# Kernel tuning notes

Measured on AMD Instinct MI355X. Metric: run time of the kernel, lower is better.

## Reference

```python
import jax, jax.numpy as jnp
import numpy as np

# Dims: B=batch, T=seq, D=input=256=F*F, H=hidden=256=F*F, F=16 factor, R=16 TT rank, 4 gates (I,F,G,O)
F, R, NG = 16, 16, 4


def setup_inputs():
    key = jax.random.key(0)
    ks = jax.random.split(key, 11)
    s = 0.1  # core init scale keeps gate pre-activations O(1)
    inp = {
        "x": jax.random.normal(ks[0], (64, 1024, 256), jnp.float32),
        # TT cores for the 4 input-to-hidden gates (boundary ranks squeezed)
        "ih_g0": s * jax.random.normal(ks[1], (NG, F, R), jnp.float32),
        "ih_g1": s * jax.random.normal(ks[2], (NG, R, F, R), jnp.float32),
        "ih_g2": s * jax.random.normal(ks[3], (NG, R, F, R), jnp.float32),
        "ih_g3": s * jax.random.normal(ks[4], (NG, R, F), jnp.float32),
        "ih_bias": jnp.zeros((NG, F * F), jnp.float32),
        # TT cores for the 4 hidden-to-hidden gates
        "hh_g0": s * jax.random.normal(ks[5], (NG, F, R), jnp.float32),
        "hh_g1": s * jax.random.normal(ks[6], (NG, R, F, R), jnp.float32),
        "hh_g2": s * jax.random.normal(ks[7], (NG, R, F, R), jnp.float32),
        "hh_g3": s * jax.random.normal(ks[8], (NG, R, F), jnp.float32),
        "hh_bias": jnp.zeros((NG, F * F), jnp.float32),
    }
    return inp


def tt_linear(x2, g0, g1, g2, g3, bias):
    # x2: [N, F*F] -> contract TT cores per gate g -> [N, NG, F*F]
    n = x2.shape[0]
    x3 = x2.reshape(n, F, F)
    t = jnp.einsum('bmn,gmr->bgnr', x3, g0)      # contract first input factor
    t = jnp.einsum('bgnr,grns->bgs', t, g1)      # contract second input factor
    t = jnp.einsum('bgs,gsot->bgot', t, g2)      # emit first output factor
    y = jnp.einsum('bgot,gtp->bgop', t, g3)      # emit second output factor
    return y.reshape(n, NG, F * F) + bias        # bias: [NG, F*F]


def reference(x, ih_g0, ih_g1, ih_g2, ih_g3, ih_bias,
              hh_g0, hh_g1, hh_g2, hh_g3, hh_bias):
    B, T, D = x.shape
    H = F * F
    # Precompute input-to-hidden gate contributions for all timesteps at once
    ih_all = tt_linear(x.reshape(B * T, D), ih_g0, ih_g1, ih_g2, ih_g3, ih_bias)
    ih_all = ih_all.reshape(B, T, NG, H).transpose(1, 0, 2, 3)  # [T,B,4,H]

    def step(carry, ih_t):
        h, c = carry
        gates = ih_t + tt_linear(h, hh_g0, hh_g1, hh_g2, hh_g3, hh_bias)
        i = jax.nn.sigmoid(gates[:, 0])
        f = jax.nn.sigmoid(gates[:, 1])
        g = jnp.tanh(gates[:, 2])
        o = jax.nn.sigmoid(gates[:, 3])
        c = f * c + i * g
        h = o * jnp.tanh(c)
        return (h, c), h

    h0 = jnp.zeros((B, H), x.dtype)
    c0 = jnp.zeros((B, H), x.dtype)
    (h, c), ys = jax.lax.scan(step, (h0, c0), ih_all)
    output = ys.transpose(1, 0, 2)  # [B,T,H]
    return output, (h, c)
```

## Files before the change

### kernel.cpp

```cpp
#include <hip/hip_runtime.h>


#define WS_A1I 0
#define WS_A1H 16384
#define WS_C2I 32768
#define WS_C2H 49152
#define WS_BIAS 65536
#define WS_T2 66560

typedef float v2f __attribute__((ext_vector_type(2)));

__device__ __forceinline__ v2f pk_fma(v2f a, v2f b, v2f c) {
    v2f d;
    asm("v_pk_fma_f32 %0, %1, %2, %3" : "=v"(d) : "v"(a), "v"(b), "v"(c));
    return d;
}

__device__ __forceinline__ void bar_lds() {
    asm volatile("s_waitcnt lgkmcnt(0)\n\ts_barrier" ::: "memory");
}

template <int CTRL>
__device__ __forceinline__ float dpp_add(float v) {
    int s = __builtin_amdgcn_update_dpp(0, __float_as_int(v), CTRL, 0xF, 0xF, true);
    return v + __int_as_float(s);
}
template <int CTRL>
__device__ __forceinline__ float dpp_bcast(float v) {
    int s = __builtin_amdgcn_update_dpp(0, __float_as_int(v), CTRL, 0xF, 0xF, true);
    return __int_as_float(s);
}

__global__ void k_compose(const float* __restrict__ g0i, const float* __restrict__ g1i,
                          const float* __restrict__ g2i, const float* __restrict__ g3i,
                          const float* __restrict__ bi,
                          const float* __restrict__ g0h, const float* __restrict__ g1h,
                          const float* __restrict__ g2h, const float* __restrict__ g3h,
                          const float* __restrict__ bh,
                          float* __restrict__ ws) {
    int id = blockIdx.x * 256 + threadIdx.x;
    if (id < 16384) {
        int g = id >> 12, s = (id >> 8) & 15, mn = id & 255;
        int m = mn >> 4, n = mn & 15;
        float aI = 0.f, aH = 0.f;
        for (int r = 0; r < 16; ++r) {
            aI += g0i[(g * 16 + m) * 16 + r] * g1i[((g * 16 + r) * 16 + n) * 16 + s];
            aH += g0h[(g * 16 + m) * 16 + r] * g1h[((g * 16 + r) * 16 + n) * 16 + s];
        }
        ws[WS_A1I + (g * 16 + s) * 256 + mn] = aI;
        ws[WS_A1H + (g * 16 + s) * 256 + mn] = aH;
    } else if (id < 32768) {
        int id2 = id - 16384;
        int g = id2 >> 12, s = (id2 >> 8) & 15, j = id2 & 255;
        int o = j >> 4, p = j & 15;
        float aI = 0.f, aH = 0.f;
        for (int t = 0; t < 16; ++t) {
            aI += g2i[((g * 16 + s) * 16 + o) * 16 + t] * g3i[(g * 16 + t) * 16 + p];
            aH += g2h[((g * 16 + s) * 16 + o) * 16 + t] * g3h[(g * 16 + t) * 16 + p];
        }
        ws[WS_C2I + (g * 16 + s) * 256 + j] = aI;
        ws[WS_C2H + (g * 16 + s) * 256 + j] = aH;
    } else if (id < 33792) {
        int id2 = id - 32768;
        ws[WS_BIAS + id2] = bi[id2] + bh[id2];
    }
}

__global__ __launch_bounds__(256, 2) void k_t2ih(const float* __restrict__ x,
                                                 const float* __restrict__ ws,
                                                 float* __restrict__ T2) {
    __shared__ __align__(16) float Xs[64 * 128];
    __shared__ __align__(16) float As[64 * 128];
    const int tid = threadIdx.x;
    const long r0 = (long)blockIdx.x * 64;
    const int ro = tid & 15;
    const int q  = tid >> 4;

    const float4* X4g = (const float4*)x;
    const float4* A4  = (const float4*)(ws + WS_A1I);
    float4* Xs4 = (float4*)Xs;
    float4* As4 = (float4*)As;

    v2f acc2[4][4];
#pragma unroll
    for (int i = 0; i < 4; ++i)
#pragma unroll
        for (int j = 0; j < 4; ++j) acc2[i][j] = (v2f){0.f, 0.f};

    for (int half = 0; half < 2; ++half) {
        __syncthreads();
#pragma unroll
        for (int k = 0; k < 8; ++k) {
            int idx = k * 256 + tid;
            int row = idx >> 5, c = idx & 31;
            int sw = (row << 5) | (c ^ ((row >> 2) & 15));
            Xs4[sw] = X4g[(r0 + row) * 64 + half * 32 + c];
            As4[sw] = A4[row * 64 + half * 32 + c];
        }
        __syncthreads();

#pragma unroll 4
        for (int mn4 = 0; mn4 < 32; ++mn4) {
            float4 a[4], xv[4];
#pragma unroll
            for (int j = 0; j < 4; ++j) {
                int row = ro * 4 + j;
                a[j] = As4[(row << 5) | (mn4 ^ ro)];
            }
#pragma unroll
            for (int i = 0; i < 4; ++i) {
                int row = q * 4 + i;
                xv[i] = Xs4[(row << 5) | (mn4 ^ q)];
            }
#pragma unroll
            for (int i = 0; i < 4; ++i)
#pragma unroll
                for (int j = 0; j < 4; ++j) {
                    acc2[i][j] = pk_fma((v2f){xv[i].x, xv[i].y},
                                        (v2f){a[j].x, a[j].y}, acc2[i][j]);
                    acc2[i][j] = pk_fma((v2f){xv[i].z, xv[i].w},
                                        (v2f){a[j].z, a[j].w}, acc2[i][j]);
                }
        }
    }
#pragma unroll
    for (int i = 0; i < 4; ++i)
#pragma unroll
        for (int j = 0; j < 4; ++j)
            T2[(r0 + q * 4 + i) * 64 + ro * 4 + j] = acc2[i][j].x + acc2[i][j].y;
}

__global__ __launch_bounds__(1024, 4) void k_lstm(const float* __restrict__ ws,
                                                  const float* __restrict__ T2,
                                                  float* __restrict__ out) {
    __shared__ __align__(16) float hS[256];
    __shared__ __align__(16) float t2hS[64];
    __shared__ __align__(16) float t2iS[2][64];

    const int tid  = threadIdx.x;
    const int w    = tid >> 6;
    const int lane = tid & 63;
    const int b    = blockIdx.x;

    const int uab = 4 * w + (lane >> 4);
    const int sub = lane & 15;
    v2f a1p[8];
    {
        const float4* A1h4 = (const float4*)(ws + WS_A1H);
#pragma unroll
        for (int kk = 0; kk < 4; ++kk) {
            float4 v = A1h4[uab * 64 + sub * 4 + kk];
            a1p[2 * kk + 0] = (v2f){v.x, v.y};
            a1p[2 * kk + 1] = (v2f){v.z, v.w};
        }
    }

    const int jj = lane >> 2;
    const int g  = lane & 3;
    const int j  = 16 * w + jj;
    v2f c2hp[8], c2ip[8];
#pragma unroll
    for (int qq = 0; qq < 4; ++qq) {
        float h0 = ws[WS_C2H + (16 * g + 4 * qq + 0) * 256 + j];
        float h1 = ws[WS_C2H + (16 * g + 4 * qq + 1) * 256 + j];
        float h2 = ws[WS_C2H + (16 * g + 4 * qq + 2) * 256 + j];
        float h3 = ws[WS_C2H + (16 * g + 4 * qq + 3) * 256 + j];
        float i0 = ws[WS_C2I + (16 * g + 4 * qq + 0) * 256 + j];
        float i1 = ws[WS_C2I + (16 * g + 4 * qq + 1) * 256 + j];
        float i2 = ws[WS_C2I + (16 * g + 4 * qq + 2) * 256 + j];
        float i3 = ws[WS_C2I + (16 * g + 4 * qq + 3) * 256 + j];
        c2hp[2 * qq + 0] = (v2f){h0, h1};
        c2hp[2 * qq + 1] = (v2f){h2, h3};
        c2ip[2 * qq + 0] = (v2f){i0, i1};
        c2ip[2 * qq + 1] = (v2f){i2, i3};
    }
    float bias = ws[WS_BIAS + g * 256 + j];
    const float am = (g == 2) ? 2.0f : 1.0f;
    const float as = 1.442695040888963f * am;

#pragma unroll
    for (int i = 0; i < 8; ++i)
        asm volatile("" : "+v"(a1p[i]), "+v"(c2hp[i]), "+v"(c2ip[i]));

    const int hw = ((jj >> 2) << 6) + (w << 2) + (jj & 3);

    float c = 0.f, h_last = 0.f;
    if (tid < 256) hS[tid] = 0.f;
    const float* T2b = T2 + (long)b * 1024 * 64;
    const float4* T2b4 = (const float4*)T2b;
    float4 preA = make_float4(0.f, 0.f, 0.f, 0.f);
    float4 preB = make_float4(0.f, 0.f, 0.f, 0.f);
    if (tid < 16) {
        ((float4*)t2iS[0])[tid] = T2b4[tid];
        preA = T2b4[16 + tid];
    }
    bar_lds();

    float* outB = out + (long)b * 1024 * 256;
    const float4* hS4 = (const float4*)hS;
    const float4* th4 = (const float4*)t2hS;

    auto body = [&](int t, float4& preW, float4& preL) {
        v2f sA = (v2f){0.f, 0.f}, sB = (v2f){0.f, 0.f};
#pragma unroll
        for (int kk = 0; kk < 4; ++kk) {
            float4 hv = hS4[kk * 16 + sub];
            sA = pk_fma((v2f){hv.x, hv.y}, a1p[2 * kk + 0], sA);
            sB = pk_fma((v2f){hv.z, hv.w}, a1p[2 * kk + 1], sB);
        }
        float tv = (sA.x + sA.y) + (sB.x + sB.y);
        if ((tid < 16) && (t + 1 < 1024))
            ((float4*)t2iS[(t + 1) & 1])[tid] = preW;
        if ((tid < 16) && (t + 2 < 1024))
            preL = T2b4[(t + 2) * 16 + tid];
        tv = dpp_add<0x111>(tv);
        tv = dpp_add<0x112>(tv);
        tv = dpp_add<0x114>(tv);
        tv = dpp_add<0x118>(tv);
        if (sub == 15) t2hS[uab] = tv;

        bar_lds();

        const float4* ti4 = (const float4*)t2iS[t & 1];
        v2f aH = (v2f){bias, 0.f}, aL = (v2f){0.f, 0.f};
#pragma unroll
        for (int qq = 0; qq < 4; ++qq) {
            float4 th = th4[g * 4 + qq];
            float4 ti = ti4[g * 4 + qq];
            aH = pk_fma((v2f){th.x, th.y}, c2hp[2 * qq + 0], aH);
            aL = pk_fma((v2f){th.z, th.w}, c2hp[2 * qq + 1], aL);
            aH = pk_fma((v2f){ti.x, ti.y}, c2ip[2 * qq + 0], aH);
            aL = pk_fma((v2f){ti.z, ti.w}, c2ip[2 * qq + 1], aL);
        }
        float acc = (aH.x + aH.y) + (aL.x + aL.y);
        float e   = __builtin_amdgcn_exp2f(as * acc);
        float act = 1.0f - am * __builtin_amdgcn_rcpf(1.0f + e);
        float gi = dpp_bcast<0x00>(act);
        float gf = dpp_bcast<0x55>(act);
        float gg = dpp_bcast<0xAA>(act);
        float go = dpp_bcast<0xFF>(act);
        c = gf * c + gi * gg;
        float e2 = __builtin_amdgcn_exp2f(2.885390081777926f * c);
        float th_ = 1.0f - 2.0f * __builtin_amdgcn_rcpf(1.0f + e2);
        float h = go * th_;
        h_last = h;
        if (g == 0) {
            hS[hw] = h;
            outB[t * 256 + j] = h;
        }

        bar_lds();
    };

    for (int t = 0; t < 1024; t += 2) {
        body(t, preA, preB);
        body(t + 1, preB, preA);
    }

    if (g == 0) {
        out[16777216 + b * 256 + j] = h_last;
        out[16777216 + 16384 + b * 256 + j] = c;
    }
}

extern "C" void kernel_launch(void* const* d_in, const int* in_sizes, int n_in,
                              void* d_out, int out_size, void* d_ws, size_t ws_size,
                              hipStream_t stream) {
    const float* x     = (const float*)d_in[0];
    const float* ih_g0 = (const float*)d_in[1];
    const float* ih_g1 = (const float*)d_in[2];
    const float* ih_g2 = (const float*)d_in[3];
    const float* ih_g3 = (const float*)d_in[4];
    const float* ih_b  = (const float*)d_in[5];
    const float* hh_g0 = (const float*)d_in[6];
    const float* hh_g1 = (const float*)d_in[7];
    const float* hh_g2 = (const float*)d_in[8];
    const float* hh_g3 = (const float*)d_in[9];
    const float* hh_b  = (const float*)d_in[10];
    float* out = (float*)d_out;
    float* ws  = (float*)d_ws;

    k_compose<<<132, 256, 0, stream>>>(ih_g0, ih_g1, ih_g2, ih_g3, ih_b,
                                       hh_g0, hh_g1, hh_g2, hh_g3, hh_b, ws);
    k_t2ih<<<1024, 256, 0, stream>>>(x, ws, ws + WS_T2);
    k_lstm<<<64, 1024, 0, stream>>>(ws, ws + WS_T2, out);
}
```

Baseline: 868.4 us.

## Restructure input projection GEMM to per-wave row tiles with uniform weight loads

Rewrites the x-by-A1 projection so each wavefront owns 64 rows, one row per lane, staging x in a padded per-wave LDS tile. Each lane holds 64 accumulators, and the weight matrix is read through wave-uniform addresses that can become scalar loads. This removes the block-wide barriers and the weight staging in LDS. The grid shrinks to 256 blocks, and the cost is heavy register pressure from 64 accumulators plus many scalar/global weight reads per k-step, which may hurt occupancy.

```diff
diff --git a/kernel.cpp b/kernel.cpp
--- a/kernel.cpp
+++ b/kernel.cpp
@@ -69,65 +69,47 @@
 __global__ __launch_bounds__(256, 2) void k_t2ih(const float* __restrict__ x,
                                                  const float* __restrict__ ws,
                                                  float* __restrict__ T2) {
-    __shared__ __align__(16) float Xs[64 * 128];
-    __shared__ __align__(16) float As[64 * 128];
-    const int tid = threadIdx.x;
-    const long r0 = (long)blockIdx.x * 64;
-    const int ro = tid & 15;
-    const int q  = tid >> 4;
+    __shared__ __align__(16) float Xc[4][64 * 66 + 8];
+    const int tid  = threadIdx.x;
+    const int wv   = tid >> 6;
+    const int lane = tid & 63;
+    const long tile = (long)blockIdx.x * 4 + wv;
+    const long r0   = tile * 64;
+    float* Xw = Xc[wv];
 
     const float4* X4g = (const float4*)x;
-    const float4* A4  = (const float4*)(ws + WS_A1I);
-    float4* Xs4 = (float4*)Xs;
-    float4* As4 = (float4*)As;
-
-    v2f acc2[4][4];
-#pragma unroll
-    for (int i = 0; i < 4; ++i)
-#pragma unroll
-        for (int j = 0; j < 4; ++j) acc2[i][j] = (v2f){0.f, 0.f};
-
-    for (int half = 0; half < 2; ++half) {
-        __syncthreads();
-#pragma unroll
-        for (int k = 0; k < 8; ++k) {
-            int idx = k * 256 + tid;
-            int row = idx >> 5, c = idx & 31;
-            int sw = (row << 5) | (c ^ ((row >> 2) & 15));
-            Xs4[sw] = X4g[(r0 + row) * 64 + half * 32 + c];
-            As4[sw] = A4[row * 64 + half * 32 + c];
-        }
-        __syncthreads();
-
-#pragma unroll 4
-        for (int mn4 = 0; mn4 < 32; ++mn4) {
-            float4 a[4], xv[4];
-#pragma unroll
-            for (int j = 0; j < 4; ++j) {
-                int row = ro * 4 + j;
-                a[j] = As4[(row << 5) | (mn4 ^ ro)];
+    const float* A = ws + WS_A1I;
+
+    float acc[64];
+#pragma unroll
+    for (int u = 0; u < 64; ++u) acc[u] = 0.f;
+
+    for (int kc = 0; kc < 4; ++kc) {
+#pragma unroll
+        for (int it = 0; it < 16; ++it) {
+            int row = it * 4 + (lane >> 4);
+            int c4  = lane & 15;
+            float4 v = X4g[(r0 + row) * 64 + kc * 16 + c4];
+            float* d = &Xw[row * 66 + c4 * 4];
+            d[0] = v.x; d[1] = v.y; d[2] = v.z; d[3] = v.w;
+        }
+        for (int kp = 0; kp < 32; ++kp) {
+            v2f xp = *(const v2f*)&Xw[lane * 66 + 2 * kp];
+            const float* Ak = A + kc * 64 + 2 * kp;
+#pragma unroll
+            for (int u = 0; u < 64; ++u) {
+                acc[u] += xp.x * Ak[u * 256] + xp.y * Ak[u * 256 + 1];
             }
-#pragma unroll
-            for (int i = 0; i < 4; ++i) {
-                int row = q * 4 + i;
-                xv[i] = Xs4[(row << 5) | (mn4 ^ q)];
-            }
-#pragma unroll
-            for (int i = 0; i < 4; ++i)
-#pragma unroll
-                for (int j = 0; j < 4; ++j) {
-                    acc2[i][j] = pk_fma((v2f){xv[i].x, xv[i].y},
-                                        (v2f){a[j].x, a[j].y}, acc2[i][j]);
-                    acc2[i][j] = pk_fma((v2f){xv[i].z, xv[i].w},
-                                        (v2f){a[j].z, a[j].w}, acc2[i][j]);
-                }
-        }
-    }
-#pragma unroll
-    for (int i = 0; i < 4; ++i)
-#pragma unroll
-        for (int j = 0; j < 4; ++j)
-            T2[(r0 + q * 4 + i) * 64 + ro * 4 + j] = acc2[i][j].x + acc2[i][j].y;
+        }
+    }
+    float4* T24 = (float4*)T2;
+#pragma unroll
+    for (int u4 = 0; u4 < 16; ++u4) {
+        float4 o;
+        o.x = acc[4 * u4 + 0]; o.y = acc[4 * u4 + 1];
+        o.z = acc[4 * u4 + 2]; o.w = acc[4 * u4 + 3];
+        T24[(r0 + lane) * 16 + u4] = o;
+    }
 }
 
 __global__ __launch_bounds__(1024, 4) void k_lstm(const float* __restrict__ ws,
@@ -282,6 +264,6 @@
 
     k_compose<<<132, 256, 0, stream>>>(ih_g0, ih_g1, ih_g2, ih_g3, ih_b,
                                        hh_g0, hh_g1, hh_g2, hh_g3, hh_b, ws);
-    k_t2ih<<<1024, 256, 0, stream>>>(x, ws, ws + WS_T2);
+    k_t2ih<<<256, 256, 0, stream>>>(x, ws, ws + WS_T2);
     k_lstm<<<64, 1024, 0, stream>>>(ws, ws + WS_T2, out);
 }
```

New measurement: 1.045 ms. 1.2x slower.

## Halve LSTM block size, give each thread two hidden units

Applied to the files above, without the earlier changes.

The recurrent LSTM kernel now runs 512 threads per block instead of 1024, and each thread handles two hidden outputs and two rank-projection rows (j and j+128, uab and uab+32). Per-thread register weights double. The point is to make the per-step barriers cheaper with fewer waves and to add instruction-level parallelism inside the serial time loop. The trade-off is more serial work per thread on the critical path and higher register pressure.

```diff
diff --git a/kernel.cpp b/kernel.cpp
--- a/kernel.cpp
+++ b/kernel.cpp
@@ -130,9 +130,9 @@
             T2[(r0 + q * 4 + i) * 64 + ro * 4 + j] = acc2[i][j].x + acc2[i][j].y;
 }
 
-__global__ __launch_bounds__(1024, 4) void k_lstm(const float* __restrict__ ws,
-                                                  const float* __restrict__ T2,
-                                                  float* __restrict__ out) {
+__global__ __launch_bounds__(512, 2) void k_lstm(const float* __restrict__ ws,
+                                                 const float* __restrict__ T2,
+                                                 float* __restrict__ out) {
     __shared__ __align__(16) float hS[256];
     __shared__ __align__(16) float t2hS[64];
     __shared__ __align__(16) float t2iS[2][64];
@@ -144,47 +144,54 @@
 
     const int uab = 4 * w + (lane >> 4);
     const int sub = lane & 15;
-    v2f a1p[8];
+    v2f a1p0[8], a1p1[8];
     {
         const float4* A1h4 = (const float4*)(ws + WS_A1H);
 #pragma unroll
         for (int kk = 0; kk < 4; ++kk) {
-            float4 v = A1h4[uab * 64 + sub * 4 + kk];
-            a1p[2 * kk + 0] = (v2f){v.x, v.y};
-            a1p[2 * kk + 1] = (v2f){v.z, v.w};
+            float4 v0 = A1h4[uab * 64 + sub * 4 + kk];
+            float4 v1 = A1h4[(uab + 32) * 64 + sub * 4 + kk];
+            a1p0[2 * kk + 0] = (v2f){v0.x, v0.y};
+            a1p0[2 * kk + 1] = (v2f){v0.z, v0.w};
+            a1p1[2 * kk + 0] = (v2f){v1.x, v1.y};
+            a1p1[2 * kk + 1] = (v2f){v1.z, v1.w};
         }
     }
 
     const int jj = lane >> 2;
     const int g  = lane & 3;
-    const int j  = 16 * w + jj;
-    v2f c2hp[8], c2ip[8];
+    const int j0 = 16 * w + jj;
+    const int j1 = j0 + 128;
+    v2f c2hp0[8], c2ip0[8], c2hp1[8], c2ip1[8];
 #pragma unroll
     for (int qq = 0; qq < 4; ++qq) {
-        float h0 = ws[WS_C2H + (16 * g + 4 * qq + 0) * 256 + j];
-        float h1 = ws[WS_C2H + (16 * g + 4 * qq + 1) * 256 + j];
-        float h2 = ws[WS_C2H + (16 * g + 4 * qq + 2) * 256 + j];
-        float h3 = ws[WS_C2H + (16 * g + 4 * qq + 3) * 256 + j];
-        float i0 = ws[WS_C2I + (16 * g + 4 * qq + 0) * 256 + j];
-        float i1 = ws[WS_C2I + (16 * g + 4 * qq + 1) * 256 + j];
-        float i2 = ws[WS_C2I + (16 * g + 4 * qq + 2) * 256 + j];
-        float i3 = ws[WS_C2I + (16 * g + 4 * qq + 3) * 256 + j];
-        c2hp[2 * qq + 0] = (v2f){h0, h1};
-        c2hp[2 * qq + 1] = (v2f){h2, h3};
-        c2ip[2 * qq + 0] = (v2f){i0, i1};
-        c2ip[2 * qq + 1] = (v2f){i2, i3};
-    }
-    float bias = ws[WS_BIAS + g * 256 + j];
+#pragma unroll
+        for (int hh = 0; hh < 2; ++hh) {
+            int s0 = 16 * g + 4 * qq + 2 * hh;
+            c2hp0[2 * qq + hh] = (v2f){ws[WS_C2H + (s0 + 0) * 256 + j0],
+                                       ws[WS_C2H + (s0 + 1) * 256 + j0]};
+            c2ip0[2 * qq + hh] = (v2f){ws[WS_C2I + (s0 + 0) * 256 + j0],
+                                       ws[WS_C2I + (s0 + 1) * 256 + j0]};
+            c2hp1[2 * qq + hh] = (v2f){ws[WS_C2H + (s0 + 0) * 256 + j1],
+                                       ws[WS_C2H + (s0 + 1) * 256 + j1]};
+            c2ip1[2 * qq + hh] = (v2f){ws[WS_C2I + (s0 + 0) * 256 + j1],
+                                       ws[WS_C2I + (s0 + 1) * 256 + j1]};
+        }
+    }
+    float bias0 = ws[WS_BIAS + g * 256 + j0];
+    float bias1 = ws[WS_BIAS + g * 256 + j1];
     const float am = (g == 2) ? 2.0f : 1.0f;
     const float as = 1.442695040888963f * am;
 
 #pragma unroll
     for (int i = 0; i < 8; ++i)
-        asm volatile("" : "+v"(a1p[i]), "+v"(c2hp[i]), "+v"(c2ip[i]));
-
-    const int hw = ((jj >> 2) << 6) + (w << 2) + (jj & 3);
-
-    float c = 0.f, h_last = 0.f;
+        asm volatile("" : "+v"(a1p0[i]), "+v"(a1p1[i]), "+v"(c2hp0[i]),
+                         "+v"(c2ip0[i]), "+v"(c2hp1[i]), "+v"(c2ip1[i]));
+
+    const int hw0 = ((jj >> 2) << 6) + 4 * w + (jj & 3);
+    const int hw1 = hw0 + 32;
+
+    float c0 = 0.f, c1 = 0.f, h0l = 0.f, h1l = 0.f;
     if (tid < 256) hS[tid] = 0.f;
     const float* T2b = T2 + (long)b * 1024 * 64;
     const float4* T2b4 = (const float4*)T2b;
@@ -201,52 +208,76 @@
     const float4* th4 = (const float4*)t2hS;
 
     auto body = [&](int t, float4& preW, float4& preL) {
-        v2f sA = (v2f){0.f, 0.f}, sB = (v2f){0.f, 0.f};
+        v2f sA0 = (v2f){0.f, 0.f}, sB0 = (v2f){0.f, 0.f};
+        v2f sA1 = (v2f){0.f, 0.f}, sB1 = (v2f){0.f, 0.f};
 #pragma unroll
         for (int kk = 0; kk < 4; ++kk) {
             float4 hv = hS4[kk * 16 + sub];
-            sA = pk_fma((v2f){hv.x, hv.y}, a1p[2 * kk + 0], sA);
-            sB = pk_fma((v2f){hv.z, hv.w}, a1p[2 * kk + 1], sB);
-        }
-        float tv = (sA.x + sA.y) + (sB.x + sB.y);
+            v2f hxy = (v2f){hv.x, hv.y}, hzw = (v2f){hv.z, hv.w};
+            sA0 = pk_fma(hxy, a1p0[2 * kk + 0], sA0);
+            sB0 = pk_fma(hzw, a1p0[2 * kk + 1], sB0);
+            sA1 = pk_fma(hxy, a1p1[2 * kk + 0], sA1);
+            sB1 = pk_fma(hzw, a1p1[2 * kk + 1], sB1);
+        }
+        float tv0 = (sA0.x + sA0.y) + (sB0.x + sB0.y);
+        float tv1 = (sA1.x + sA1.y) + (sB1.x + sB1.y);
         if ((tid < 16) && (t + 1 < 1024))
             ((float4*)t2iS[(t + 1) & 1])[tid] = preW;
         if ((tid < 16) && (t + 2 < 1024))
             preL = T2b4[(t + 2) * 16 + tid];
-        tv = dpp_add<0x111>(tv);
-        tv = dpp_add<0x112>(tv);
-        tv = dpp_add<0x114>(tv);
-        tv = dpp_add<0x118>(tv);
-        if (sub == 15) t2hS[uab] = tv;
+        tv0 = dpp_add<0x111>(tv0);  tv1 = dpp_add<0x111>(tv1);
+        tv0 = dpp_add<0x112>(tv0);  tv1 = dpp_add<0x112>(tv1);
+        tv0 = dpp_add<0x114>(tv0);  tv1 = dpp_add<0x114>(tv1);
+        tv0 = dpp_add<0x118>(tv0);  tv1 = dpp_add<0x118>(tv1);
+        if (sub == 15) {
+            t2hS[uab]      = tv0;
+            t2hS[uab + 32] = tv1;
+        }
 
         bar_lds();
 
         const float4* ti4 = (const float4*)t2iS[t & 1];
-        v2f aH = (v2f){bias, 0.f}, aL = (v2f){0.f, 0.f};
+        v2f aH0 = (v2f){bias0, 0.f}, aL0 = (v2f){0.f, 0.f};
+        v2f aH1 = (v2f){bias1, 0.f}, aL1 = (v2f){0.f, 0.f};
 #pragma unroll
         for (int qq = 0; qq < 4; ++qq) {
             float4 th = th4[g * 4 + qq];
             float4 ti = ti4[g * 4 + qq];
-            aH = pk_fma((v2f){th.x, th.y}, c2hp[2 * qq + 0], aH);
-            aL = pk_fma((v2f){th.z, th.w}, c2hp[2 * qq + 1], aL);
-            aH = pk_fma((v2f){ti.x, ti.y}, c2ip[2 * qq + 0], aH);
-            aL = pk_fma((v2f){ti.z, ti.w}, c2ip[2 * qq + 1], aL);
-        }
-        float acc = (aH.x + aH.y) + (aL.x + aL.y);
-        float e   = __builtin_amdgcn_exp2f(as * acc);
-        float act = 1.0f - am * __builtin_amdgcn_rcpf(1.0f + e);
-        float gi = dpp_bcast<0x00>(act);
-        float gf = dpp_bcast<0x55>(act);
-        float gg = dpp_bcast<0xAA>(act);
-        float go = dpp_bcast<0xFF>(act);
-        c = gf * c + gi * gg;
-        float e2 = __builtin_amdgcn_exp2f(2.885390081777926f * c);
-        float th_ = 1.0f - 2.0f * __builtin_amdgcn_rcpf(1.0f + e2);
-        float h = go * th_;
-        h_last = h;
+            v2f txy = (v2f){th.x, th.y}, tzw = (v2f){th.z, th.w};
+            v2f ixy = (v2f){ti.x, ti.y}, izw = (v2f){ti.z, ti.w};
+            aH0 = pk_fma(txy, c2hp0[2 * qq + 0], aH0);
+            aL0 = pk_fma(tzw, c2hp0[2 * qq + 1], aL0);
+            aH1 = pk_fma(txy, c2hp1[2 * qq + 0], aH1);
+            aL1 = pk_fma(tzw, c2hp1[2 * qq + 1], aL1);
+            aH0 = pk_fma(ixy, c2ip0[2 * qq + 0], aH0);
+            aL0 = pk_fma(izw, c2ip0[2 * qq + 1], aL0);
+            aH1 = pk_fma(ixy, c2ip1[2 * qq + 0], aH1);
+            aL1 = pk_fma(izw, c2ip1[2 * qq + 1], aL1);
+        }
+        float acc0 = (aH0.x + aH0.y) + (aL0.x + aL0.y);
+        float acc1 = (aH1.x + aH1.y) + (aL1.x + aL1.y);
+        float e0   = __builtin_amdgcn_exp2f(as * acc0);
+        float e1   = __builtin_amdgcn_exp2f(as * acc1);
+        float act0 = 1.0f - am * __builtin_amdgcn_rcpf(1.0f + e0);
+        float act1 = 1.0f - am * __builtin_amdgcn_rcpf(1.0f + e1);
+        float gi0 = dpp_bcast<0x00>(act0), gi1 = dpp_bcast<0x00>(act1);
+        float gf0 = dpp_bcast<0x55>(act0), gf1 = dpp_bcast<0x55>(act1);
+        float gg0 = dpp_bcast<0xAA>(act0), gg1 = dpp_bcast<0xAA>(act1);
+        float go0 = dpp_bcast<0xFF>(act0), go1 = dpp_bcast<0xFF>(act1);
+        c0 = gf0 * c0 + gi0 * gg0;
+        c1 = gf1 * c1 + gi1 * gg1;
+        float ex0 = __builtin_amdgcn_exp2f(2.885390081777926f * c0);
+        float ex1 = __builtin_amdgcn_exp2f(2.885390081777926f * c1);
+        float th0 = 1.0f - 2.0f * __builtin_amdgcn_rcpf(1.0f + ex0);
+        float th1 = 1.0f - 2.0f * __builtin_amdgcn_rcpf(1.0f + ex1);
+        float h0 = go0 * th0;
+        float h1 = go1 * th1;
+        h0l = h0; h1l = h1;
         if (g == 0) {
-            hS[hw] = h;
-            outB[t * 256 + j] = h;
+            hS[hw0] = h0;
+            hS[hw1] = h1;
+            outB[t * 256 + j0] = h0;
+            outB[t * 256 + j1] = h1;
         }
 
         bar_lds();
@@ -258,8 +289,10 @@
     }
 
     if (g == 0) {
-        out[16777216 + b * 256 + j] = h_last;
-        out[16777216 + 16384 + b * 256 + j] = c;
+        out[16777216 + b * 256 + j0] = h0l;
+        out[16777216 + b * 256 + j1] = h1l;
+        out[16777216 + 16384 + b * 256 + j0] = c0;
+        out[16777216 + 16384 + b * 256 + j1] = c1;
     }
 }
 
@@ -283,5 +316,5 @@
     k_compose<<<132, 256, 0, stream>>>(ih_g0, ih_g1, ih_g2, ih_g3, ih_b,
                                        hh_g0, hh_g1, hh_g2, hh_g3, hh_b, ws);
     k_t2ih<<<1024, 256, 0, stream>>>(x, ws, ws + WS_T2);
-    k_lstm<<<64, 1024, 0, stream>>>(ws, ws + WS_T2, out);
-}
+    k_lstm<<<64, 512, 0, stream>>>(ws, ws + WS_T2, out);
+}
```

Measured after the change: 845.0 us. 2.7% less time.
